# Kernel optimization log

Hardware: AMD Instinct MI355X
Metric: run time of the kernel (lower is better)

## Reference

```python
import jax, jax.numpy as jnp
import numpy as np

N_NODES = 100000
N_EDGES = 3200000


def gcn_conv(x, src, dst, W, b, n_nodes):
    # symmetric normalization with self-loops already appended to src/dst
    deg = jax.ops.segment_sum(jnp.ones_like(dst, dtype=x.dtype), dst, num_segments=n_nodes)
    dis = jnp.where(deg > 0, jax.lax.rsqrt(jnp.maximum(deg, 1.0)), 0.0)  # deg^-1/2
    norm = dis[src] * dis[dst]                       # [E']
    h = x @ W                                        # [N, d_out]
    msg = h[src] * norm[:, None]                     # [E', d_out]
    out = jax.ops.segment_sum(msg, dst, num_segments=n_nodes)
    return out + b


def setup_inputs() -> dict:
    key = jax.random.key(0)
    k1, k2, k3, k4 = jax.random.split(key, 4)
    x = jax.random.normal(k1, (N_NODES, 512), dtype=jnp.float32)
    edge_index = jax.random.randint(k2, (2, N_EDGES), 0, N_NODES, dtype=jnp.int32)
    W1 = jax.random.normal(k3, (512, 256), dtype=jnp.float32) * (1.0 / np.sqrt(512))
    b1 = jnp.zeros((256,), dtype=jnp.float32)
    W2 = jax.random.normal(k4, (256, 64), dtype=jnp.float32) * (1.0 / np.sqrt(256))
    b2 = jnp.zeros((64,), dtype=jnp.float32)
    return {"x": x, "edge_index": edge_index, "W1": W1, "b1": b1, "W2": W2, "b2": b2}


def reference(x, edge_index, W1, b1, W2, b2):
    n = x.shape[0]
    loops = jnp.arange(n, dtype=edge_index.dtype)
    src = jnp.concatenate([edge_index[0], loops])  # add self-loops (GCNConv default)
    dst = jnp.concatenate([edge_index[1], loops])
    # CRD: GCNConv -> relu (dropout is identity at inference)
    h = jax.nn.relu(gcn_conv(x, src, dst, W1, b1, n))
    # CLS: GCNConv -> log_softmax over classes
    out = jax.nn.log_softmax(gcn_conv(h, src, dst, W2, b2, n), axis=1)
    return out
```

## Files before the change

kernel.cpp:

```cpp
#include <hip/hip_runtime.h>
#include <hip/hip_bf16.h>
#include <math.h>

#define TB 256

typedef __attribute__((ext_vector_type(8))) short bf16x8;
typedef __attribute__((ext_vector_type(4))) float f32x4;
typedef __attribute__((ext_vector_type(2))) float f32x2;

__device__ inline float bf2f(ushort u) {
    union { uint u; float f; } c; c.u = ((uint)u) << 16; return c.f;
}
__device__ inline ushort f2bf(float f) {
    __hip_bfloat16 h = __float2bfloat16(f);
    union { __hip_bfloat16 h; ushort u; } c; c.h = h; return c.u;
}
__device__ inline float i2f(int i) { union { int i; float f; } c; c.i = i; return c.f; }
__device__ inline int f2i(float f) { union { float f; int i; } c; c.f = f; return c.i; }


#if __has_builtin(__builtin_amdgcn_cvt_pk_fp8_f32) && __has_builtin(__builtin_amdgcn_cvt_pk_f32_fp8)
#define FP8_HW 1
#endif

__device__ inline unsigned char f2fp8(float v) {
#ifdef FP8_HW
    unsigned int r = __builtin_amdgcn_cvt_pk_fp8_f32(v, v, 0u, false);
    return (unsigned char)(r & 0xffu);
#else
    unsigned int s = (v < 0.f) ? 0x80u : 0u;
    float a = fabsf(v);
    if (a >= 448.f) return (unsigned char)(s | 0x7E);
    if (a < 0.015625f) {
        int m = (int)(a * 512.f + 0.5f);
        if (m >= 8) return (unsigned char)(s | 0x08);
        return (unsigned char)(s | m);
    }
    int e; float fr = frexpf(a, &e);
    int m = (int)(fr * 16.f + 0.5f) - 8;
    int E = e + 6;
    if (m == 8) { m = 0; E += 1; }
    if (E >= 16) return (unsigned char)(s | 0x7E);
    return (unsigned char)(s | (E << 3) | m);
#endif
}

#ifndef FP8_HW
__device__ inline float fp8_to_f(unsigned int b) {
    unsigned int s = (b & 0x80u) << 24;
    unsigned int e = (b >> 3) & 0xFu;
    unsigned int m = b & 7u;
    if (e == 0) { float val = (float)m * 0.001953125f; return s ? -val : val; }
    union { unsigned int u; float f; } c;
    c.u = s | ((e + 120u) << 23) | (m << 20);
    return c.f;
}
#endif

__device__ inline void fp8x4_fma(unsigned int v, float w, float4& acc) {
#ifdef FP8_HW
    f32x2 lo = __builtin_amdgcn_cvt_pk_f32_fp8(v, false);
    f32x2 hi = __builtin_amdgcn_cvt_pk_f32_fp8(v, true);
    acc.x = fmaf(lo.x, w, acc.x);
    acc.y = fmaf(lo.y, w, acc.y);
    acc.z = fmaf(hi.x, w, acc.z);
    acc.w = fmaf(hi.y, w, acc.w);
#else
    acc.x = fmaf(fp8_to_f(v & 0xff), w, acc.x);
    acc.y = fmaf(fp8_to_f((v >> 8) & 0xff), w, acc.y);
    acc.z = fmaf(fp8_to_f((v >> 16) & 0xff), w, acc.z);
    acc.w = fmaf(fp8_to_f(v >> 24), w, acc.w);
#endif
}

__device__ inline float fp8_dec1(unsigned int b) {
#ifdef FP8_HW
    f32x2 lo = __builtin_amdgcn_cvt_pk_f32_fp8(b & 0xffu, false);
    return lo.x;
#else
    return fp8_to_f(b & 0xffu);
#endif
}


__global__ __launch_bounds__(256) void k_setup(const float* __restrict__ W1, ushort* __restrict__ W1T,
                                               const float* __restrict__ W2, ushort* __restrict__ W2T,
                                               int* __restrict__ bhist) {
    int b = blockIdx.x;
    int t = threadIdx.x;
    if (b < 512) {
        int id = b * 256 + t;
        int k = id >> 8, nn = id & 255;
        W1T[(size_t)nn * 512 + k] = f2bf(W1[id]);
    } else if (b < 576) {
        int id = (b - 512) * 256 + t;
        int k = id >> 6, nn = id & 63;
        W2T[(size_t)nn * 256 + k] = f2bf(W2[id]);
    } else {
        bhist[t] = 0;
    }
}


__global__ __launch_bounds__(256) void k_bhist(const int* __restrict__ dst, int E,
                                               int* __restrict__ hist) {
    __shared__ int lh[256];
    int t = threadIdx.x;
    lh[t] = 0;
    __syncthreads();
    for (int e = blockIdx.x * blockDim.x + t; e < E; e += gridDim.x * blockDim.x)
        atomicAdd(&lh[dst[e] >> 9], 1);
    __syncthreads();
    if (lh[t]) atomicAdd(&hist[t], lh[t]);
}

__global__ __launch_bounds__(256) void k_bscan(const int* __restrict__ hist,
                                               int* __restrict__ bcur,
                                               int* __restrict__ bbase) {
    __shared__ int sh[256];
    int t = threadIdx.x;
    int v = hist[t];
    sh[t] = v;
    __syncthreads();
    for (int off = 1; off < 256; off <<= 1) {
        int u = (t >= off) ? sh[t - off] : 0;
        __syncthreads();
        sh[t] += u;
        __syncthreads();
    }
    int excl = sh[t] - v;
    bcur[t]  = excl;
    bbase[t] = excl;
}

__global__ __launch_bounds__(256) void k_partition(const int* __restrict__ src,
                                                   const int* __restrict__ dst, int E,
                                                   int* __restrict__ bcur,
                                                   int2* __restrict__ sorted) {
    __shared__ int  lcnt[256];
    __shared__ int  pr[256];
    __shared__ int  lbase[256];
    __shared__ int  gbase[256];
    __shared__ int  lcur[256];
    __shared__ int2 lsort[8192];

    const int per = 8192;
    const int e0 = blockIdx.x * per;
    const int e1 = min(E, e0 + per);
    const int m  = e1 - e0;
    const int t  = threadIdx.x;

    lcnt[t] = 0;
    __syncthreads();
    for (int e = e0 + t; e < e1; e += 256)
        atomicAdd(&lcnt[dst[e] >> 9], 1);
    __syncthreads();

    int v = lcnt[t];
    pr[t] = v;
    __syncthreads();
    for (int off = 1; off < 256; off <<= 1) {
        int u = (t >= off) ? pr[t - off] : 0;
        __syncthreads();
        pr[t] += u;
        __syncthreads();
    }
    int excl = pr[t] - v;
    lbase[t] = excl;
    lcur[t]  = excl;
    gbase[t] = v ? atomicAdd(&bcur[t], v) : 0;
    __syncthreads();

    for (int e = e0 + t; e < e1; e += 256) {
        int d = dst[e], s = src[e];
        int lpos = atomicAdd(&lcur[d >> 9], 1);
        lsort[lpos] = make_int2(s, d);
    }
    __syncthreads();

    for (int j = t; j < m; j += 256) {
        int2 p = lsort[j];
        int b = p.y >> 9;
        sorted[gbase[b] + (j - lbase[b])] = p;
    }
}


__global__ __launch_bounds__(256) void k_bucket_deg(const int2* __restrict__ sorted, int E,
                                                    const int* __restrict__ bbase,
                                                    int* __restrict__ deg,
                                                    int* __restrict__ offsets,
                                                    float* __restrict__ dis, int n) {
    __shared__ int cnt[512];
    __shared__ int pr[256];
    const int b = blockIdx.x;
    const int t = threadIdx.x;
    const int bstart = bbase[b];
    const int bend   = (b < 255) ? bbase[b + 1] : E;
    const int node0  = b << 9;

    cnt[t] = 0; cnt[t + 256] = 0;
    __syncthreads();
    for (int e = bstart + t; e < bend; e += 256)
        atomicAdd(&cnt[sorted[e].y & 511], 1);
    __syncthreads();

    int c0 = cnt[2 * t], c1 = cnt[2 * t + 1];
    pr[t] = c0 + c1;
    __syncthreads();
    for (int off = 1; off < 256; off <<= 1) {
        int u = (t >= off) ? pr[t - off] : 0;
        __syncthreads();
        pr[t] += u;
        __syncthreads();
    }
    int excl = pr[t] - (c0 + c1);

    int i0 = node0 + 2 * t, i1 = i0 + 1;
    if (i0 < n) {
        deg[i0] = c0 + 1;
        offsets[i0] = bstart + excl;
        dis[i0] = rsqrtf((float)(c0 + 1));
    }
    if (i1 < n) {
        deg[i1] = c1 + 1;
        offsets[i1] = bstart + excl + c0;
        dis[i1] = rsqrtf((float)(c1 + 1));
    }
}

__global__ __launch_bounds__(256) void k_bucket_fill(const int2* __restrict__ sorted, int E,
                                                     const int* __restrict__ bbase,
                                                     const int* __restrict__ offsets,
                                                     const float* __restrict__ dis,
                                                     int2* __restrict__ csr_p, int n) {
    __shared__ int cur[512];
    const int b = blockIdx.x;
    const int t = threadIdx.x;
    const int bstart = bbase[b];
    const int bend   = (b < 255) ? bbase[b + 1] : E;
    const int node0  = b << 9;

    int i0 = node0 + t, i1 = i0 + 256;
    cur[t]       = (i0 < n) ? offsets[i0] : 0;
    cur[t + 256] = (i1 < n) ? offsets[i1] : 0;
    __syncthreads();

    for (int e = bstart + t; e < bend; e += 256) {
        int2 p = sorted[e];
        int pos = atomicAdd(&cur[p.y & 511], 1);
        csr_p[pos] = make_int2(p.x, f2i(dis[p.x]));
    }
}


__global__ __launch_bounds__(256) void k_gemm1(const float* __restrict__ A,
                                               const ushort* __restrict__ BT,
                                               unsigned char* __restrict__ C,
                                               int M, int N, int K) {
    const int BM = 64, BK = 32;
    __shared__ ushort Al[2][BM][40];
    __shared__ ushort Bl[2][256][40];

    const int t    = threadIdx.x;
    const int lane = t & 63;
    const int wid  = t >> 6;
    const int m0   = blockIdx.x * BM;
    const int lr   = lane & 15;
    const int lg   = lane >> 4;

    const int arow = t >> 2, aq = t & 3;
    const int agm  = min(m0 + arow, M - 1);
    const bool avalid = (m0 + arow) < M;

    f32x4 acc[4][4] = {};

    {
        ushort4 o0 = {0,0,0,0}, o1 = {0,0,0,0};
        if (avalid) {
            const float* ap = A + (size_t)agm * K + aq * 8;
            float4 u = *(const float4*)ap;
            float4 w = *(const float4*)(ap + 4);
            o0.x = f2bf(u.x); o0.y = f2bf(u.y); o0.z = f2bf(u.z); o0.w = f2bf(u.w);
            o1.x = f2bf(w.x); o1.y = f2bf(w.y); o1.z = f2bf(w.z); o1.w = f2bf(w.w);
        }
        *(ushort4*)(&Al[0][arow][aq * 8])     = o0;
        *(ushort4*)(&Al[0][arow][aq * 8 + 4]) = o1;
        #pragma unroll
        for (int it = 0; it < 4; ++it) {
            int c = t + it * 256;
            int row = c >> 2, q = c & 3;
            uint4 v = *(const uint4*)(BT + (size_t)row * K + q * 8);
            *(uint4*)(&Bl[0][row][q * 8]) = v;
        }
    }
    __syncthreads();

    int buf = 0;
    for (int k0 = 0; k0 < K; k0 += BK) {
        if (k0 + BK < K) {
            int nb = buf ^ 1;
            int kn = k0 + BK;
            ushort4 o0 = {0,0,0,0}, o1 = {0,0,0,0};
            if (avalid) {
                const float* ap = A + (size_t)agm * K + kn + aq * 8;
                float4 u = *(const float4*)ap;
                float4 w = *(const float4*)(ap + 4);
                o0.x = f2bf(u.x); o0.y = f2bf(u.y); o0.z = f2bf(u.z); o0.w = f2bf(u.w);
                o1.x = f2bf(w.x); o1.y = f2bf(w.y); o1.z = f2bf(w.z); o1.w = f2bf(w.w);
            }
            *(ushort4*)(&Al[nb][arow][aq * 8])     = o0;
            *(ushort4*)(&Al[nb][arow][aq * 8 + 4]) = o1;
            #pragma unroll
            for (int it = 0; it < 4; ++it) {
                int c = t + it * 256;
                int row = c >> 2, q = c & 3;
                uint4 v = *(const uint4*)(BT + (size_t)row * K + kn + q * 8);
                *(uint4*)(&Bl[nb][row][q * 8]) = v;
            }
        }

        bf16x8 fa[4], fb[4];
        #pragma unroll
        for (int mi = 0; mi < 4; ++mi)
            fa[mi] = *(const bf16x8*)(&Al[buf][mi * 16 + lr][lg * 8]);
        #pragma unroll
        for (int ni = 0; ni < 4; ++ni)
            fb[ni] = *(const bf16x8*)(&Bl[buf][wid * 64 + ni * 16 + lr][lg * 8]);
        #pragma unroll
        for (int mi = 0; mi < 4; ++mi)
            #pragma unroll
            for (int ni = 0; ni < 4; ++ni)
                acc[mi][ni] = __builtin_amdgcn_mfma_f32_16x16x32_bf16(fa[mi], fb[ni], acc[mi][ni], 0, 0, 0);
        __syncthreads();
        buf ^= 1;
    }

    #pragma unroll
    for (int mi = 0; mi < 4; ++mi) {
        int rbase = m0 + mi * 16 + lg * 4;
        #pragma unroll
        for (int v = 0; v < 4; ++v) {
            int gm = rbase + v;
            if (gm < M) {
                #pragma unroll
                for (int ni = 0; ni < 4; ++ni)
                    C[(size_t)gm * N + wid * 64 + ni * 16 + lr] = f2fp8(acc[mi][ni][v]);
            }
        }
    }
}


__device__ inline uint relu_pk(uint u) {
    uint lo = u & 0x0000FFFFu;
    uint hi = u & 0xFFFF0000u;
    if (u & 0x00008000u) lo = 0;
    if (u & 0x80000000u) hi = 0;
    return lo | hi;
}

__global__ __launch_bounds__(256) void k_gemm2(const ushort* __restrict__ A,
                                               const ushort* __restrict__ BT,
                                               unsigned char* __restrict__ C,
                                               int M, int N, int K) {
    const int BM = 128, BK = 32;
    __shared__ ushort Al[BM][40];
    __shared__ ushort Bl[64][40];

    const int t    = threadIdx.x;
    const int lane = t & 63;
    const int wid  = t >> 6;
    const int wm   = wid >> 1, wn = wid & 1;
    const int m0   = blockIdx.x * BM;
    const int lr   = lane & 15;
    const int lg   = lane >> 4;

    f32x4 acc[4][2] = {};

    for (int k0 = 0; k0 < K; k0 += BK) {
        #pragma unroll
        for (int i = 0; i < 2; ++i) {
            int c = t + i * 256;
            int row = c >> 2, q = c & 3;
            int gm = m0 + row;
            uint4 v = make_uint4(0, 0, 0, 0);
            if (gm < M) v = *(const uint4*)(A + (size_t)gm * K + k0 + q * 8);
            v.x = relu_pk(v.x); v.y = relu_pk(v.y); v.z = relu_pk(v.z); v.w = relu_pk(v.w);
            *(uint4*)(&Al[row][q * 8]) = v;
        }
        {
            int row = t >> 2, q = t & 3;
            uint4 v = *(const uint4*)(BT + (size_t)(row) * K + k0 + q * 8);
            *(uint4*)(&Bl[row][q * 8]) = v;
        }
        __syncthreads();

        bf16x8 fa[4], fb[2];
        #pragma unroll
        for (int mi = 0; mi < 4; ++mi)
            fa[mi] = *(const bf16x8*)(&Al[wm * 64 + mi * 16 + lr][lg * 8]);
        #pragma unroll
        for (int ni = 0; ni < 2; ++ni)
            fb[ni] = *(const bf16x8*)(&Bl[wn * 32 + ni * 16 + lr][lg * 8]);
        #pragma unroll
        for (int mi = 0; mi < 4; ++mi)
            #pragma unroll
            for (int ni = 0; ni < 2; ++ni)
                acc[mi][ni] = __builtin_amdgcn_mfma_f32_16x16x32_bf16(fa[mi], fb[ni], acc[mi][ni], 0, 0, 0);
        __syncthreads();
    }

    #pragma unroll
    for (int mi = 0; mi < 4; ++mi) {
        int rbase = m0 + wm * 64 + mi * 16 + lg * 4;
        #pragma unroll
        for (int v = 0; v < 4; ++v) {
            int gm = rbase + v;
            if (gm < M) {
                #pragma unroll
                for (int ni = 0; ni < 2; ++ni)
                    C[(size_t)gm * N + wn * 32 + ni * 16 + lr] = f2fp8(acc[mi][ni][v]);
            }
        }
    }
}


__global__ __launch_bounds__(256) void k_agg256(const unsigned char* __restrict__ h,
                                                const int2* __restrict__ csr_p,
                                                const int* __restrict__ off,
                                                const int* __restrict__ deg,
                                                const float* __restrict__ dis,
                                                const float* __restrict__ bias,
                                                ushort* __restrict__ out, int n) {
    int wave = (int)((blockIdx.x * (size_t)blockDim.x + threadIdx.x) >> 6);
    int lane = threadIdx.x & 63;
    if (wave >= n) return;
    const int i = wave;
    const float di = dis[i];
    const int beg = off[i], cnt = deg[i] - 1, end = beg + cnt;

    float4 bv = ((const float4*)bias)[lane];
    unsigned int hv = ((const unsigned int*)(h + (size_t)i * 256))[lane];
    float sl = di * di;
    float4 a0 = bv, a1 = {0,0,0,0}, a2 = {0,0,0,0}, a3 = {0,0,0,0};
    fp8x4_fma(hv, sl, a0);

    for (int base = beg; base < end; base += 64) {
        int m = end - base; if (m > 64) m = 64;
        int2 p = (lane < m) ? csr_p[base + lane] : make_int2(0, 0);
        int   msrc = p.x;
        float mw   = (lane < m) ? i2f(p.y) * di : 0.f;
        int k = 0;
        for (; k + 4 <= m; k += 4) {
            int s0 = __shfl(msrc, k),     s1 = __shfl(msrc, k + 1);
            int s2 = __shfl(msrc, k + 2), s3 = __shfl(msrc, k + 3);
            float w0 = __shfl(mw, k),     w1 = __shfl(mw, k + 1);
            float w2 = __shfl(mw, k + 2), w3 = __shfl(mw, k + 3);
            unsigned int v0 = ((const unsigned int*)(h + (size_t)s0 * 256))[lane];
            unsigned int v1 = ((const unsigned int*)(h + (size_t)s1 * 256))[lane];
            unsigned int v2 = ((const unsigned int*)(h + (size_t)s2 * 256))[lane];
            unsigned int v3 = ((const unsigned int*)(h + (size_t)s3 * 256))[lane];
            fp8x4_fma(v0, w0, a0);
            fp8x4_fma(v1, w1, a1);
            fp8x4_fma(v2, w2, a2);
            fp8x4_fma(v3, w3, a3);
        }
        for (; k < m; ++k) {
            int   s0 = __shfl(msrc, k); float w0 = __shfl(mw, k);
            unsigned int v0 = ((const unsigned int*)(h + (size_t)s0 * 256))[lane];
            fp8x4_fma(v0, w0, a0);
        }
    }
    ushort4 o;
    o.x = f2bf((a0.x + a1.x) + (a2.x + a3.x));
    o.y = f2bf((a0.y + a1.y) + (a2.y + a3.y));
    o.z = f2bf((a0.z + a1.z) + (a2.z + a3.z));
    o.w = f2bf((a0.w + a1.w) + (a2.w + a3.w));
    ((ushort4*)(out + (size_t)i * 256))[lane] = o;
}


__global__ __launch_bounds__(256) void k_agg64_lsm(const unsigned char* __restrict__ h,
                                                   const int2* __restrict__ csr_p,
                                                   const int* __restrict__ off,
                                                   const int* __restrict__ deg,
                                                   const float* __restrict__ dis,
                                                   const float* __restrict__ bias,
                                                   float* __restrict__ out, int n) {
    int wave = (int)((blockIdx.x * (size_t)blockDim.x + threadIdx.x) >> 6);
    int lane = threadIdx.x & 63;
    if (wave >= n) return;
    const int i = wave;
    const float di = dis[i];
    const int beg = off[i], cnt = deg[i] - 1, end = beg + cnt;

    float a0 = fmaf(fp8_dec1(h[(size_t)i * 64 + lane]), di * di, bias[lane]);
    float a1 = 0.f, a2 = 0.f, a3 = 0.f;

    for (int base = beg; base < end; base += 64) {
        int m = end - base; if (m > 64) m = 64;
        int2 p = (lane < m) ? csr_p[base + lane] : make_int2(0, 0);
        int   msrc = p.x;
        float mw   = (lane < m) ? i2f(p.y) * di : 0.f;
        int k = 0;
        for (; k + 4 <= m; k += 4) {
            int s0 = __shfl(msrc, k),     s1 = __shfl(msrc, k + 1);
            int s2 = __shfl(msrc, k + 2), s3 = __shfl(msrc, k + 3);
            float w0 = __shfl(mw, k),     w1 = __shfl(mw, k + 1);
            float w2 = __shfl(mw, k + 2), w3 = __shfl(mw, k + 3);
            a0 = fmaf(fp8_dec1(h[(size_t)s0 * 64 + lane]), w0, a0);
            a1 = fmaf(fp8_dec1(h[(size_t)s1 * 64 + lane]), w1, a1);
            a2 = fmaf(fp8_dec1(h[(size_t)s2 * 64 + lane]), w2, a2);
            a3 = fmaf(fp8_dec1(h[(size_t)s3 * 64 + lane]), w3, a3);
        }
        for (; k < m; ++k) {
            int s0 = __shfl(msrc, k); float w0 = __shfl(mw, k);
            a0 = fmaf(fp8_dec1(h[(size_t)s0 * 64 + lane]), w0, a0);
        }
    }
    float v = (a0 + a1) + (a2 + a3);

    float mx = v;
    #pragma unroll
    for (int o = 32; o > 0; o >>= 1) mx = fmaxf(mx, __shfl_xor(mx, o));
    float ex = __expf(v - mx);
    float ssum = ex;
    #pragma unroll
    for (int o = 32; o > 0; o >>= 1) ssum += __shfl_xor(ssum, o);
    out[(size_t)i * 64 + lane] = v - mx - logf(ssum);
}


extern "C" void kernel_launch(void* const* d_in, const int* in_sizes, int n_in,
                              void* d_out, int out_size, void* d_ws, size_t ws_size,
                              hipStream_t stream) {
    const float* x  = (const float*)d_in[0];
    const int*   ei = (const int*)d_in[1];
    const float* W1 = (const float*)d_in[2];
    const float* b1 = (const float*)d_in[3];
    const float* W2 = (const float*)d_in[4];
    const float* b2 = (const float*)d_in[5];
    float* out = (float*)d_out;

    const int n = in_sizes[0] / 512;
    const int E = in_sizes[1] / 2;
    const int* src = ei;
    const int* dst = ei + E;

    char* ws = (char*)d_ws;
    int*    deg     = (int*)(ws + 0);
    float*  dis     = (float*)(ws + 400000);
    int*    offsets = (int*)(ws + 800000);
    int*    bhist   = (int*)(ws + 1200000);
    int*    bcur    = (int*)(ws + 1201024);
    int*    bbase   = (int*)(ws + 1202048);
    int2*   csr_p   = (int2*)(ws + 1203072);
    ushort* W1T     = (ushort*)(ws + 26803072);
    ushort* W2T     = (ushort*)(ws + 27065216);
    unsigned char* h1 = (unsigned char*)(ws + 27097984);
    ushort* out1    = (ushort*)(ws + 52697984);
    unsigned char* h2 = (unsigned char*)(ws + 103897984);
    int2*   sorted  = (int2*)(ws + 110297984);

    const int PB   = (E + 8191) / 8192;
    const int NBKT = (n + 511) / 512;

    k_setup<<<577, 256, 0, stream>>>(W1, W1T, W2, W2T, bhist);

    k_bhist<<<512, 256, 0, stream>>>(dst, E, bhist);
    k_bscan<<<1, 256, 0, stream>>>(bhist, bcur, bbase);
    k_partition<<<PB, 256, 0, stream>>>(src, dst, E, bcur, sorted);

    k_bucket_deg<<<NBKT, 256, 0, stream>>>(sorted, E, bbase, deg, offsets, dis, n);
    k_bucket_fill<<<NBKT, 256, 0, stream>>>(sorted, E, bbase, offsets, dis, csr_p, n);

    k_gemm1<<<(n + 63) / 64, TB, 0, stream>>>(x, W1T, h1, n, 256, 512);

    k_agg256<<<(n + 3) / 4, TB, 0, stream>>>(h1, csr_p, offsets, deg, dis, b1, out1, n);

    k_gemm2<<<(n + 127) / 128, TB, 0, stream>>>(out1, W2T, h2, n, 64, 256);

    k_agg64_lsm<<<(n + 3) / 4, TB, 0, stream>>>(h2, csr_p, offsets, deg, dis, b2, out, n);
}
```

Baseline: 416.5 us.

## Pack sorted edges and CSR entries into 32-bit words with quantized weights

The partition buffer now stores each edge as one 32-bit word (source shifted by 9 bits plus the low destination bits) instead of an int2. The CSR entries become one 32-bit word holding a 17-bit source index and a 15-bit fixed-point dis[src] value, which halves the traffic in the sort, fill and both aggregation kernels. The risks are lower precision on the normalization weights and a hard limit of 2^17 node indices, which 100000 nodes fits under. Workspace offsets are shifted to match the smaller buffers.

```diff
diff --git a/kernel.cpp b/kernel.cpp
--- a/kernel.cpp
+++ b/kernel.cpp
@@ -15,8 +15,6 @@
     __hip_bfloat16 h = __float2bfloat16(f);
     union { __hip_bfloat16 h; ushort u; } c; c.h = h; return c.u;
 }
-__device__ inline float i2f(int i) { union { int i; float f; } c; c.i = i; return c.f; }
-__device__ inline int f2i(float f) { union { float f; int i; } c; c.f = f; return c.i; }
 
 
 #if __has_builtin(__builtin_amdgcn_cvt_pk_fp8_f32) && __has_builtin(__builtin_amdgcn_cvt_pk_f32_fp8)
@@ -136,7 +134,7 @@
 __global__ __launch_bounds__(256) void k_partition(const int* __restrict__ src,
                                                    const int* __restrict__ dst, int E,
                                                    int* __restrict__ bcur,
-                                                   int2* __restrict__ sorted) {
+                                                   unsigned int* __restrict__ sorted) {
     __shared__ int  lcnt[256];
     __shared__ int  pr[256];
     __shared__ int  lbase[256];
@@ -181,12 +179,12 @@
     for (int j = t; j < m; j += 256) {
         int2 p = lsort[j];
         int b = p.y >> 9;
-        sorted[gbase[b] + (j - lbase[b])] = p;
-    }
-}
-
-
-__global__ __launch_bounds__(256) void k_bucket_deg(const int2* __restrict__ sorted, int E,
+        sorted[gbase[b] + (j - lbase[b])] = ((unsigned int)p.x << 9) | (unsigned int)(p.y & 511);
+    }
+}
+
+
+__global__ __launch_bounds__(256) void k_bucket_deg(const unsigned int* __restrict__ sorted, int E,
                                                     const int* __restrict__ bbase,
                                                     int* __restrict__ deg,
                                                     int* __restrict__ offsets,
@@ -202,7 +200,7 @@
     cnt[t] = 0; cnt[t + 256] = 0;
     __syncthreads();
     for (int e = bstart + t; e < bend; e += 256)
-        atomicAdd(&cnt[sorted[e].y & 511], 1);
+        atomicAdd(&cnt[sorted[e] & 511u], 1);
     __syncthreads();
 
     int c0 = cnt[2 * t], c1 = cnt[2 * t + 1];
@@ -229,11 +227,11 @@
     }
 }
 
-__global__ __launch_bounds__(256) void k_bucket_fill(const int2* __restrict__ sorted, int E,
+__global__ __launch_bounds__(256) void k_bucket_fill(const unsigned int* __restrict__ sorted, int E,
                                                      const int* __restrict__ bbase,
                                                      const int* __restrict__ offsets,
                                                      const float* __restrict__ dis,
-                                                     int2* __restrict__ csr_p, int n) {
+                                                     unsigned int* __restrict__ csr_p, int n) {
     __shared__ int cur[512];
     const int b = blockIdx.x;
     const int t = threadIdx.x;
@@ -247,9 +245,11 @@
     __syncthreads();
 
     for (int e = bstart + t; e < bend; e += 256) {
-        int2 p = sorted[e];
-        int pos = atomicAdd(&cur[p.y & 511], 1);
-        csr_p[pos] = make_int2(p.x, f2i(dis[p.x]));
+        unsigned int p = sorted[e];
+        int s = (int)(p >> 9);
+        int pos = atomicAdd(&cur[p & 511u], 1);
+        unsigned int dq = (unsigned int)(dis[s] * 32767.0f + 0.5f);
+        csr_p[pos] = ((unsigned int)s << 15) | dq;
     }
 }
 
@@ -428,7 +428,7 @@
 
 
 __global__ __launch_bounds__(256) void k_agg256(const unsigned char* __restrict__ h,
-                                                const int2* __restrict__ csr_p,
+                                                const unsigned int* __restrict__ csr_p,
                                                 const int* __restrict__ off,
                                                 const int* __restrict__ deg,
                                                 const float* __restrict__ dis,
@@ -439,6 +439,7 @@
     if (wave >= n) return;
     const int i = wave;
     const float di = dis[i];
+    const float dscale = di * (1.0f / 32767.0f);
     const int beg = off[i], cnt = deg[i] - 1, end = beg + cnt;
 
     float4 bv = ((const float4*)bias)[lane];
@@ -449,9 +450,9 @@
 
     for (int base = beg; base < end; base += 64) {
         int m = end - base; if (m > 64) m = 64;
-        int2 p = (lane < m) ? csr_p[base + lane] : make_int2(0, 0);
-        int   msrc = p.x;
-        float mw   = (lane < m) ? i2f(p.y) * di : 0.f;
+        unsigned int p = (lane < m) ? csr_p[base + lane] : 0u;
+        int   msrc = (int)(p >> 15);
+        float mw   = (float)(p & 0x7fffu) * dscale;
         int k = 0;
         for (; k + 4 <= m; k += 4) {
             int s0 = __shfl(msrc, k),     s1 = __shfl(msrc, k + 1);
@@ -483,7 +484,7 @@
 
 
 __global__ __launch_bounds__(256) void k_agg64_lsm(const unsigned char* __restrict__ h,
-                                                   const int2* __restrict__ csr_p,
+                                                   const unsigned int* __restrict__ csr_p,
                                                    const int* __restrict__ off,
                                                    const int* __restrict__ deg,
                                                    const float* __restrict__ dis,
@@ -494,6 +495,7 @@
     if (wave >= n) return;
     const int i = wave;
     const float di = dis[i];
+    const float dscale = di * (1.0f / 32767.0f);
     const int beg = off[i], cnt = deg[i] - 1, end = beg + cnt;
 
     float a0 = fmaf(fp8_dec1(h[(size_t)i * 64 + lane]), di * di, bias[lane]);
@@ -501,9 +503,9 @@
 
     for (int base = beg; base < end; base += 64) {
         int m = end - base; if (m > 64) m = 64;
-        int2 p = (lane < m) ? csr_p[base + lane] : make_int2(0, 0);
-        int   msrc = p.x;
-        float mw   = (lane < m) ? i2f(p.y) * di : 0.f;
+        unsigned int p = (lane < m) ? csr_p[base + lane] : 0u;
+        int   msrc = (int)(p >> 15);
+        float mw   = (float)(p & 0x7fffu) * dscale;
         int k = 0;
         for (; k + 4 <= m; k += 4) {
             int s0 = __shfl(msrc, k),     s1 = __shfl(msrc, k + 1);
@@ -556,13 +558,13 @@
     int*    bhist   = (int*)(ws + 1200000);
     int*    bcur    = (int*)(ws + 1201024);
     int*    bbase   = (int*)(ws + 1202048);
-    int2*   csr_p   = (int2*)(ws + 1203072);
-    ushort* W1T     = (ushort*)(ws + 26803072);
-    ushort* W2T     = (ushort*)(ws + 27065216);
-    unsigned char* h1 = (unsigned char*)(ws + 27097984);
-    ushort* out1    = (ushort*)(ws + 52697984);
-    unsigned char* h2 = (unsigned char*)(ws + 103897984);
-    int2*   sorted  = (int2*)(ws + 110297984);
+    unsigned int* csr_p = (unsigned int*)(ws + 1203072);
+    ushort* W1T     = (ushort*)(ws + 14003072);
+    ushort* W2T     = (ushort*)(ws + 14265216);
+    unsigned char* h1 = (unsigned char*)(ws + 14297984);
+    ushort* out1    = (ushort*)(ws + 39897984);
+    unsigned char* h2 = (unsigned char*)(ws + 91097984);
+    unsigned int* sorted = (unsigned int*)(ws + 97497984);
 
     const int PB   = (E + 8191) / 8192;
     const int NBKT = (n + 511) / 512;
```

Measured after the change: 413.7 us. No clear change (-0.7%).
